# Kernel optimization log

Measured on AMD Instinct MI355X. Metric: run time of the kernel, lower is better.

## Reference

```python
import jax, jax.numpy as jnp
import numpy as np

HEAD_NUM = 16
EMBED_DIM = 512


def setup_inputs() -> dict:
    key = jax.random.key(0)
    k1, k2, k3, k4, k5 = jax.random.split(key, 5)
    B, N, D = 8, 2048, EMBED_DIM
    x = jax.random.normal(k1, (B, N, D), dtype=jnp.float32)
    dis_matrix = jax.random.uniform(k2, (B, N, N), dtype=jnp.float32)
    s = 1.0 / np.sqrt(D)
    Wq = jax.random.normal(k3, (D, D), dtype=jnp.float32) * s
    Wk = jax.random.normal(k4, (D, D), dtype=jnp.float32) * s
    Wv = jax.random.normal(k5, (D, D), dtype=jnp.float32) * s
    alpha = jnp.float32(1.0)
    return {"x": x, "dis_matrix": dis_matrix, "Wq": Wq, "Wk": Wk, "Wv": Wv, "alpha": alpha}


def _split_heads(t, H):
    # [B, N, D] -> [B, H, N, D//H]
    B, N, D = t.shape
    return t.reshape(B, N, H, D // H).transpose(0, 2, 1, 3)


def reference(x, dis_matrix, Wq, Wk, Wv, alpha):
    B, N, D = x.shape
    H = HEAD_NUM
    # nn.Linear(bias=False): y = x @ W.T
    q = _split_heads(x @ Wq.T, H)  # [B,H,N,dk]
    k = _split_heads(x @ Wk.T, H)
    v = _split_heads(x @ Wv.T, H)
    log2n = jnp.float32(np.log2(N))
    dis_weight = jnp.exp(-alpha * log2n * dis_matrix)  # [B,N,N]
    k_weight = jnp.exp(k)
    # contract over source node i -> target node j
    weight_1 = jnp.einsum('bij,bhik->bhjk', dis_weight, k_weight * v)
    weight_2 = jnp.einsum('bij,bhik->bhjk', dis_weight, k_weight)
    out = jax.nn.sigmoid(q) * (weight_1 / weight_2)  # [B,H,N,dk]
    return out.transpose(0, 2, 1, 3).reshape(B, N, D)
```

## Files before the change

### kernel.cpp

```cpp
#include <hip/hip_runtime.h>
#include <math.h>
#include <stdint.h>


typedef __bf16 bf16_t;
typedef __attribute__((ext_vector_type(4))) __bf16 bf16x4;
typedef __attribute__((ext_vector_type(8))) __bf16 bf16x8;
typedef __attribute__((ext_vector_type(4))) float f32x4;

#define MFMA_BF16(a, b, c) __builtin_amdgcn_mfma_f32_16x16x32_bf16((a), (b), (c), 0, 0, 0)

static __device__ __forceinline__ void async_ld16(const bf16_t* g, bf16_t* lds) {
  __builtin_amdgcn_global_load_lds(
      reinterpret_cast<__attribute__((address_space(1))) unsigned int*>(
          reinterpret_cast<uintptr_t>(g)),
      reinterpret_cast<__attribute__((address_space(3))) unsigned int*>(
          reinterpret_cast<uintptr_t>(lds)),
      16, 0, 0);
}

template <int ROWS>
static __device__ __forceinline__ void stage3(const bf16_t* g, int ldg, bf16_t* lds,
                                              int wv, int lane) {
  const int r_in = lane >> 3;
  const int cpos = lane & 7;
#pragma unroll
  for (int s = 0; s < ROWS / 32; ++s) {
    int rbase = wv * (ROWS / 4) + s * 8;
    int row = rbase + r_in;
    int cg = cpos ^ (row & 7);
    async_ld16(g + (size_t)row * ldg + cg * 8, lds + rbase * 64 + lane * 8);
  }
}

static __device__ __forceinline__ bf16x8 frag3(const bf16_t* lds, int row16,
                                               int l15, int quad, int kc) {
  int p = (quad | (kc << 2)) ^ (l15 & 7);
  return *(const bf16x8*)&lds[(row16 + l15) * 64 + p * 8];
}

__global__ __launch_bounds__(256) void cvt_all(const float* __restrict__ x,
                                               const float* __restrict__ wq,
                                               const float* __restrict__ wk,
                                               const float* __restrict__ wv,
                                               bf16_t* __restrict__ xb,
                                               bf16_t* __restrict__ wall) {
  int i = blockIdx.x * 256 + threadIdx.x;
  if (i >= 2293760) return;
  const float* src;
  bf16_t* dst;
  int off;
  if (i < 2097152) {
    src = x; dst = xb; off = i;
  } else {
    int j = i - 2097152;
    int sel = j >> 16;
    off = j & 65535;
    src = (sel == 0) ? wq : (sel == 1) ? wk : wv;
    dst = wall + (size_t)sel * 262144;
  }
  f32x4 f = ((const f32x4*)src)[off];
  bf16x4 o;
  o[0] = (bf16_t)f[0]; o[1] = (bf16_t)f[1]; o[2] = (bf16_t)f[2]; o[3] = (bf16_t)f[3];
  ((bf16x4*)dst)[off] = o;
}

__global__ __launch_bounds__(256, 4) void proj_dw(const bf16_t* __restrict__ A,
                                                  const bf16_t* __restrict__ W,
                                                  bf16_t* __restrict__ qs,
                                                  bf16_t* __restrict__ kwT,
                                                  bf16_t* __restrict__ kwvT,
                                                  const float* __restrict__ dis,
                                                  bf16_t* __restrict__ dwT,
                                                  const float* __restrict__ alpha) {
  __shared__ __align__(16) char pool[32768];
  const int tid = threadIdx.x;
  const int idx = blockIdx.x;
  const int g19 = idx / 19, r19 = idx % 19;

  if (r19 >= 3) {
    int sub = g19 * 16 + (r19 - 3);
    int jt = sub & 31, it = (sub >> 5) & 31, b = sub >> 10;
    bf16_t* t = (bf16_t*)pool;
    const float coef = -alpha[0] * 11.0f;
    const int j0 = jt * 64, i0 = it * 64;
    const int rr = tid >> 4, cc = (tid & 15) * 4;
#pragma unroll
    for (int p = 0; p < 4; ++p) {
      int i = rr + p * 16;
      f32x4 d = *(const f32x4*)&dis[((size_t)(b * 2048 + i0 + i)) * 2048 + j0 + cc];
#pragma unroll
      for (int e = 0; e < 4; ++e) t[(cc + e) * 65 + i] = (bf16_t)__expf(coef * d[e]);
    }
    __syncthreads();
#pragma unroll
    for (int p = 0; p < 4; ++p) {
      int j = rr + p * 16;
      bf16x4 o;
#pragma unroll
      for (int e = 0; e < 4; ++e) o[e] = t[j * 65 + cc + e];
      *(bf16x4*)&dwT[((size_t)(b * 2048 + j0 + j)) * 2048 + i0 + cc] = o;
    }
    return;
  }

  const int sub = g19 * 3 + r19;
  const int m_blk = sub / 12, n_blk = sub % 12;
  bf16_t* As = (bf16_t*)pool;
  const int K = 512;
  const int wv = tid >> 6, lane = tid & 63;
  const int l15 = lane & 15, quad = lane >> 4;
  const int wm = wv >> 1, wn = wv & 1;
  const bf16_t* Am = A + (size_t)(m_blk * 128) * K;
  const int b = m_blk >> 4;

  if (n_blk < 4) {
    bf16_t* Bsq = (bf16_t*)(pool + 16384);
    const int c_loc = n_blk * 128;
    f32x4 acc[4][4];
#pragma unroll
    for (int a = 0; a < 4; ++a)
#pragma unroll
      for (int c = 0; c < 4; ++c) acc[a][c] = (f32x4){0.f, 0.f, 0.f, 0.f};

    for (int k0 = 0; k0 < K; k0 += 64) {
      stage3<128>(Am + k0, K, As, wv, lane);
      stage3<128>(W + (size_t)c_loc * K + k0, K, Bsq, wv, lane);
      __syncthreads();
#pragma unroll
      for (int kc = 0; kc < 2; ++kc) {
        bf16x8 a[4], bb[4];
#pragma unroll
        for (int mf = 0; mf < 4; ++mf) a[mf] = frag3(As, wm * 64 + mf * 16, l15, quad, kc);
#pragma unroll
        for (int nf = 0; nf < 4; ++nf) bb[nf] = frag3(Bsq, wn * 64 + nf * 16, l15, quad, kc);
#pragma unroll
        for (int mf = 0; mf < 4; ++mf)
#pragma unroll
          for (int nf = 0; nf < 4; ++nf) acc[mf][nf] = MFMA_BF16(a[mf], bb[nf], acc[mf][nf]);
      }
      __syncthreads();
    }
#pragma unroll
    for (int mf = 0; mf < 4; ++mf)
#pragma unroll
      for (int nf = 0; nf < 4; ++nf) {
        int j16 = (m_blk & 15) * 8 + wm * 4 + mf;
        int c16 = n_blk * 8 + wn * 4 + nf;
        bf16x4 o;
#pragma unroll
        for (int r = 0; r < 4; ++r)
          o[r] = (bf16_t)(1.0f / (1.0f + __expf(-acc[mf][nf][r])));
        size_t off = (((size_t)b * 128 + j16) * 32 + c16) * 256 + quad * 64 + l15 * 4;
        *(bf16x4*)&qs[off] = o;
      }
  } else {
    bf16_t* Bk = (bf16_t*)(pool + 16384);
    bf16_t* Bv = (bf16_t*)(pool + 24576);
    const int c_loc = (n_blk - 4) * 64;
    f32x4 acck[4][2], accv[4][2];
#pragma unroll
    for (int a = 0; a < 4; ++a)
#pragma unroll
      for (int c = 0; c < 2; ++c) {
        acck[a][c] = (f32x4){0.f, 0.f, 0.f, 0.f};
        accv[a][c] = (f32x4){0.f, 0.f, 0.f, 0.f};
      }
    const bf16_t* Wk = W + (size_t)(512 + c_loc) * K;
    const bf16_t* Wv = W + (size_t)(1024 + c_loc) * K;

    for (int k0 = 0; k0 < K; k0 += 64) {
      stage3<128>(Am + k0, K, As, wv, lane);
      stage3<64>(Wk + k0, K, Bk, wv, lane);
      stage3<64>(Wv + k0, K, Bv, wv, lane);
      __syncthreads();
#pragma unroll
      for (int kc = 0; kc < 2; ++kc) {
        bf16x8 a[4], bk[2], bv[2];
#pragma unroll
        for (int mf = 0; mf < 4; ++mf) a[mf] = frag3(As, wm * 64 + mf * 16, l15, quad, kc);
#pragma unroll
        for (int nf = 0; nf < 2; ++nf) {
          bk[nf] = frag3(Bk, wn * 32 + nf * 16, l15, quad, kc);
          bv[nf] = frag3(Bv, wn * 32 + nf * 16, l15, quad, kc);
        }
#pragma unroll
        for (int mf = 0; mf < 4; ++mf)
#pragma unroll
          for (int nf = 0; nf < 2; ++nf) {
            acck[mf][nf] = MFMA_BF16(a[mf], bk[nf], acck[mf][nf]);
            accv[mf][nf] = MFMA_BF16(a[mf], bv[nf], accv[mf][nf]);
          }
      }
      __syncthreads();
    }

    bf16_t* Lk = (bf16_t*)pool;
    bf16_t* Lv = (bf16_t*)(pool + 8704);
    const int t0 = (m_blk * 128) & 2047;
#pragma unroll
    for (int ci = 0; ci < 2; ++ci) {
      if (wn == ci) {
#pragma unroll
        for (int mf = 0; mf < 4; ++mf)
#pragma unroll
          for (int nf = 0; nf < 2; ++nf) {
            int cl = nf * 16 + l15;
            int tl = wm * 64 + mf * 16 + quad * 4;
#pragma unroll
            for (int r = 0; r < 4; ++r) {
              float kw = __expf(acck[mf][nf][r]);
              Lk[cl * 136 + tl + r] = (bf16_t)kw;
              Lv[cl * 136 + tl + r] = (bf16_t)(kw * accv[mf][nf][r]);
            }
          }
      }
      __syncthreads();
      {
        int rowt = tid >> 3, colt = (tid & 7) * 16;
        int c = c_loc + ci * 32 + rowt;
        size_t g = ((size_t)b * 512 + c) * 2048 + t0 + colt;
        *(bf16x8*)&kwT[g] = *(const bf16x8*)&Lk[rowt * 136 + colt];
        *(bf16x8*)&kwT[g + 8] = *(const bf16x8*)&Lk[rowt * 136 + colt + 8];
        *(bf16x8*)&kwvT[g] = *(const bf16x8*)&Lv[rowt * 136 + colt];
        *(bf16x8*)&kwvT[g + 8] = *(const bf16x8*)&Lv[rowt * 136 + colt + 8];
      }
      __syncthreads();
    }
  }
}

__global__ __launch_bounds__(512, 2) void main_gemm(const bf16_t* __restrict__ dwT,
                                                    const bf16_t* __restrict__ kwvT,
                                                    const bf16_t* __restrict__ kwT,
                                                    const bf16_t* __restrict__ qs,
                                                    float* __restrict__ out) {
  extern __shared__ __align__(16) char smem_raw[];
  bf16_t* const lds = (bf16_t*)smem_raw;
  const int K = 2048;
  const int tid = threadIdx.x;
  const int wv = tid >> 6, lane = tid & 63;
  const int l15 = lane & 15, quad = lane >> 4;
  const int bi = blockIdx.x;
  const int b = bi & 7, nbb = (bi >> 3) & 3, mb = bi >> 5;
  const int wm = wv >> 2, wn = wv & 3;
  const int r_in = lane >> 3, cpos = lane & 7;
  const int cg = cpos ^ r_in;

  const bf16_t* const Ab = dwT + ((size_t)b * 2048 + mb * 256) * K;
  const bf16_t* const BvB = kwvT + (size_t)b * 512 * K;
  const bf16_t* const BkB = kwT + (size_t)b * 512 * K;

  const bf16_t* aSrc[4];
  const bf16_t* bSrc[4];
#pragma unroll
  for (int s = 0; s < 4; ++s) {
    const int row = s * 64 + wv * 8 + r_in;
    aSrc[s] = Ab + (size_t)row * K + cg * 8;
    const int type = (row >> 4) & 1;
    const int crow = nbb * 128 + (row >> 5) * 16 + (row & 15);
    const bf16_t* base = type ? BkB : BvB;
    bSrc[s] = base + (size_t)crow * K + cg * 8;
  }

  f32x4 acc[8][4];
#pragma unroll
  for (int m = 0; m < 8; ++m)
#pragma unroll
    for (int n = 0; n < 4; ++n) acc[m][n] = (f32x4){0.f, 0.f, 0.f, 0.f};

  bf16x8 a[8];
  bf16x8 b0[4];
  bf16x8 b1[4];

#define STAGE_T(dst, koff)                                                         \
  do {                                                                             \
    bf16_t* A_ = lds + (dst)*32768;                                                \
    _Pragma("unroll") for (int s = 0; s < 4; ++s)                                  \
        async_ld16(aSrc[s] + (koff), A_ + s * 4096 + wv * 512 + lane * 8);         \
    _Pragma("unroll") for (int s = 0; s < 4; ++s)                                  \
        async_ld16(bSrc[s] + (koff), A_ + 16384 + s * 4096 + wv * 512 + lane * 8); \
  } while (0)

#define LOADA(As_, mh)                                                             \
  do {                                                                             \
    _Pragma("unroll") for (int mf = 0; mf < 4; ++mf)                               \
        _Pragma("unroll") for (int kc = 0; kc < 2; ++kc)                           \
            a[mf * 2 + kc] =                                                       \
        frag3((As_), wm * 128 + (mh)*64 + mf * 16, l15, quad, kc);                 \
  } while (0)

#define LOADB(Bs_, dstarr, nh)                                                     \
  do {                                                                             \
    _Pragma("unroll") for (int nf = 0; nf < 2; ++nf)                               \
        _Pragma("unroll") for (int kc = 0; kc < 2; ++kc)                           \
            dstarr[nf * 2 + kc] =                                                  \
        frag3((Bs_), wn * 64 + (nh)*32 + nf * 16, l15, quad, kc);                  \
  } while (0)

#define MFMA_PH(mh, nh, barr)                                                      \
  do {                                                                             \
    __builtin_amdgcn_s_setprio(1);                                                 \
    _Pragma("unroll") for (int kc = 0; kc < 2; ++kc)                               \
        _Pragma("unroll") for (int mf = 0; mf < 4; ++mf)                           \
            _Pragma("unroll") for (int nf = 0; nf < 2; ++nf)                       \
                acc[(mh)*4 + mf][(nh)*2 + nf] =                                    \
        MFMA_BF16(a[mf * 2 + kc], barr[nf * 2 + kc], acc[(mh)*4 + mf][(nh)*2 + nf]); \
    __builtin_amdgcn_s_setprio(0);                                                 \
  } while (0)

  STAGE_T(0, 0);
  __syncthreads();

  for (int t = 0; t < 32; ++t) {
    const int c = t & 1;
    const bf16_t* As_c = lds + c * 32768;
    const bf16_t* Bs_c = As_c + 16384;
    if (t < 31) STAGE_T(c ^ 1, (t + 1) * 64);
    LOADA(As_c, 0);
    LOADB(Bs_c, b0, 0);
    __builtin_amdgcn_s_barrier();
    MFMA_PH(0, 0, b0);
    __builtin_amdgcn_s_barrier();
    LOADB(Bs_c, b1, 1);
    __builtin_amdgcn_s_barrier();
    MFMA_PH(0, 1, b1);
    __builtin_amdgcn_s_barrier();
    LOADA(As_c, 1);
    __builtin_amdgcn_s_barrier();
    MFMA_PH(1, 1, b1);
    __builtin_amdgcn_s_barrier();
    MFMA_PH(1, 0, b0);
    __syncthreads();
  }

#undef STAGE_T
#undef LOADA
#undef LOADB
#undef MFMA_PH

#pragma unroll
  for (int mf = 0; mf < 8; ++mf)
#pragma unroll
    for (int p = 0; p < 2; ++p) {
      f32x4 w1 = acc[mf][2 * p];
      f32x4 w2 = acc[mf][2 * p + 1];
      const int j16 = mb * 16 + wm * 8 + mf;
      const int c16 = nbb * 8 + wn * 2 + p;
      size_t qoff = (((size_t)b * 128 + j16) * 32 + c16) * 256 + quad * 64 + l15 * 4;
      bf16x4 qv = *(const bf16x4*)&qs[qoff];
      const int ccol = c16 * 16 + l15;
#pragma unroll
      for (int r = 0; r < 4; ++r) {
        const int j = j16 * 16 + quad * 4 + r;
        out[((size_t)b * 2048 + j) * 512 + ccol] = (float)qv[r] * (w1[r] / w2[r]);
      }
    }
}

extern "C" void kernel_launch(void* const* d_in, const int* in_sizes, int n_in,
                              void* d_out, int out_size, void* d_ws, size_t ws_size,
                              hipStream_t stream) {
  const float* x = (const float*)d_in[0];
  const float* dis = (const float*)d_in[1];
  const float* Wq = (const float*)d_in[2];
  const float* Wk = (const float*)d_in[3];
  const float* Wv = (const float*)d_in[4];
  const float* alpha = (const float*)d_in[5];
  float* out = (float*)d_out;

  char* p = (char*)d_ws;
  bf16_t* x_bf = (bf16_t*)p;  p += (size_t)16384 * 512 * 2;
  bf16_t* Wall = (bf16_t*)p;  p += (size_t)1536 * 512 * 2;
  bf16_t* kwT  = (bf16_t*)p;  p += (size_t)8 * 512 * 2048 * 2;
  bf16_t* kwvT = (bf16_t*)p;  p += (size_t)8 * 512 * 2048 * 2;
  bf16_t* dwT  = (bf16_t*)p;  p += (size_t)8 * 2048 * 2048 * 2;
  bf16_t* qs_bf = (bf16_t*)p; p += (size_t)16384 * 512 * 2;
  if ((size_t)(p - (char*)d_ws) > ws_size) return;

  static bool attr_done = false;
  if (!attr_done) {
    hipFuncSetAttribute(reinterpret_cast<const void*>(main_gemm),
                        hipFuncAttributeMaxDynamicSharedMemorySize, 131072);
    attr_done = true;
  }

  cvt_all<<<8960, 256, 0, stream>>>(x, Wq, Wk, Wv, x_bf, Wall);
  proj_dw<<<9728, 256, 0, stream>>>(x_bf, Wall, qs_bf, kwT, kwvT, dis, dwT, alpha);
  main_gemm<<<256, 512, 131072, stream>>>(dwT, kwvT, kwT, qs_bf, out);
}
```

Before: 313.7 us.

## Split next-tile prefetch into phases with partial vmcnt waits instead of full syncs

Splits the double-buffered global-to-LDS prefetch of the next K tile into three groups, issued between the MFMA phases of the current tile. The B rows are remapped so each group holds exactly the fragments the next phase needs. The end-of-iteration __syncthreads, which drains every outstanding load, is replaced by s_waitcnt vmcnt(N) plus s_barrier, so each wave waits only for the chunk it is about to read. The aim is to overlap global memory latency with MFMA work. The cost is fragile hand-written waitcnt accounting that has to match the exact issue order of the async loads.

Result: no change. 308.6 us (median of 2 runs) (-1.6%).

```diff
diff --git a/kernel.cpp b/kernel.cpp
--- a/kernel.cpp
+++ b/kernel.cpp
@@ -18,6 +18,12 @@
           reinterpret_cast<uintptr_t>(lds)),
       16, 0, 0);
 }
+
+#define WAITV(N)                                          \
+  do {                                                    \
+    asm volatile("s_waitcnt vmcnt(" #N ")" ::: "memory"); \
+    __builtin_amdgcn_sched_barrier(0);                    \
+  } while (0)
 
 template <int ROWS>
 static __device__ __forceinline__ void stage3(const bf16_t* g, int ldg, bf16_t* lds,
@@ -252,15 +258,24 @@
   const bf16_t* const BkB = kwT + (size_t)b * 512 * K;
 
   const bf16_t* aSrc[4];
-  const bf16_t* bSrc[4];
+  int aDst[4];
 #pragma unroll
   for (int s = 0; s < 4; ++s) {
     const int row = s * 64 + wv * 8 + r_in;
     aSrc[s] = Ab + (size_t)row * K + cg * 8;
+    aDst[s] = s * 4096 + wv * 512 + lane * 8;
+  }
+  const bf16_t* bSrc[4];
+  int bDst[4];
+#pragma unroll
+  for (int cb = 0; cb < 4; ++cb) {
+    const int base1 = (cb & 1) * 128 + (cb >> 1) * 32;
+    const int rowbase = base1 + (wv >> 2) * 64 + (wv & 3) * 8;
+    const int row = rowbase + r_in;
     const int type = (row >> 4) & 1;
     const int crow = nbb * 128 + (row >> 5) * 16 + (row & 15);
-    const bf16_t* base = type ? BkB : BvB;
-    bSrc[s] = base + (size_t)crow * K + cg * 8;
+    bSrc[cb] = (type ? BkB : BvB) + (size_t)crow * K + cg * 8;
+    bDst[cb] = 16384 + rowbase * 64 + lane * 8;
   }
 
   f32x4 acc[8][4];
@@ -273,14 +288,8 @@
   bf16x8 b0[4];
   bf16x8 b1[4];
 
-#define STAGE_T(dst, koff)                                                         \
-  do {                                                                             \
-    bf16_t* A_ = lds + (dst)*32768;                                                \
-    _Pragma("unroll") for (int s = 0; s < 4; ++s)                                  \
-        async_ld16(aSrc[s] + (koff), A_ + s * 4096 + wv * 512 + lane * 8);         \
-    _Pragma("unroll") for (int s = 0; s < 4; ++s)                                  \
-        async_ld16(bSrc[s] + (koff), A_ + 16384 + s * 4096 + wv * 512 + lane * 8); \
-  } while (0)
+#define STAGE_A(dst, s, koff) async_ld16(aSrc[s] + (koff), lds + (dst)*32768 + aDst[s])
+#define STAGE_B(dst, cb, koff) async_ld16(bSrc[cb] + (koff), lds + (dst)*32768 + bDst[cb])
 
 #define LOADA(As_, mh)                                                             \
   do {                                                                             \
@@ -309,32 +318,47 @@
     __builtin_amdgcn_s_setprio(0);                                                 \
   } while (0)
 
-  STAGE_T(0, 0);
-  __syncthreads();
+  STAGE_A(0, 0, 0); STAGE_A(0, 2, 0); STAGE_B(0, 0, 0); STAGE_B(0, 1, 0);
+  STAGE_B(0, 2, 0); STAGE_B(0, 3, 0); STAGE_A(0, 1, 0); STAGE_A(0, 3, 0);
+  WAITV(4);
+  __builtin_amdgcn_s_barrier();
 
   for (int t = 0; t < 32; ++t) {
     const int c = t & 1;
+    const int nx = c ^ 1;
     const bf16_t* As_c = lds + c * 32768;
     const bf16_t* Bs_c = As_c + 16384;
-    if (t < 31) STAGE_T(c ^ 1, (t + 1) * 64);
+    const int ko = (t + 1) * 64;
+    if (t < 31) { STAGE_A(nx, 0, ko); STAGE_A(nx, 2, ko); STAGE_B(nx, 0, ko); STAGE_B(nx, 1, ko); }
     LOADA(As_c, 0);
     LOADB(Bs_c, b0, 0);
     __builtin_amdgcn_s_barrier();
     MFMA_PH(0, 0, b0);
-    __builtin_amdgcn_s_barrier();
+    WAITV(6);
+    __builtin_amdgcn_s_barrier();
+    if (t < 31) { STAGE_B(nx, 2, ko); STAGE_B(nx, 3, ko); }
     LOADB(Bs_c, b1, 1);
     __builtin_amdgcn_s_barrier();
     MFMA_PH(0, 1, b1);
-    __builtin_amdgcn_s_barrier();
+    WAITV(6);
+    __builtin_amdgcn_s_barrier();
+    if (t < 31) { STAGE_A(nx, 1, ko); STAGE_A(nx, 3, ko); }
     LOADA(As_c, 1);
     __builtin_amdgcn_s_barrier();
     MFMA_PH(1, 1, b1);
     __builtin_amdgcn_s_barrier();
     MFMA_PH(1, 0, b0);
-    __syncthreads();
-  }
-
-#undef STAGE_T
+    if (t < 30) {
+      WAITV(4);
+      __builtin_amdgcn_s_barrier();
+    } else if (t == 30) {
+      WAITV(0);
+      __builtin_amdgcn_s_barrier();
+    }
+  }
+
+#undef STAGE_A
+#undef STAGE_B
 #undef LOADA
 #undef LOADB
 #undef MFMA_PH
```
